# Kernel tuning notes

Hardware: AMD Instinct MI355X
Metric: run time of the kernel (lower is better)

The kernel has to match this reference:

```python
import jax, jax.numpy as jnp
import numpy as np

B, S, DM, DE, H, DH, DC, DCq, DR = 4, 2048, 1024, 1024, 16, 64, 128, 128, 32
SCALE = 1.0 / np.sqrt(DH + DR)


def _rope_tables(seq_len, dim, theta=10000.0):
    inv = 1.0 / (theta ** (jnp.arange(0, dim, 2, dtype=jnp.float32) / dim))  # [dim/2]
    t = jnp.arange(seq_len, dtype=jnp.float32)
    ang = t[:, None] * inv[None, :]  # [S, dim/2]
    return jnp.cos(ang), jnp.sin(ang)


def _apply_rope(xq, xk, cos, sin):
    # xq, xk: [B, S, H, DR]; complex rotary on (even, odd) pairs
    def rot(x):
        s = x.shape
        xr = x.reshape(*s[:-1], s[-1] // 2, 2)
        r, i = xr[..., 0], xr[..., 1]
        c = cos[None, :s[1], None, :]
        sn = sin[None, :s[1], None, :]
        out = jnp.stack([r * c - i * sn, r * sn + i * c], axis=-1)
        return out.reshape(s)
    return rot(xq), rot(xk)


def setup_inputs() -> dict:
    key = jax.random.key(0)
    ks = jax.random.split(key, 10)
    def lin(k, din, dout):
        return 0.02 * jax.random.normal(k, (din, dout), jnp.float32)
    inp = {
        "x": jax.random.normal(ks[0], (B, S, DM), jnp.float32),
        "mask": jnp.tril(jnp.ones((S, S), jnp.float32))[None, None],
        "W_dkv": lin(ks[1], DM, DC),  "b_dkv": jnp.zeros((DC,), jnp.float32),
        "W_dq":  lin(ks[2], DM, DCq), "b_dq":  jnp.zeros((DCq,), jnp.float32),
        "W_uk":  lin(ks[3], DC, DE),  "b_uk":  jnp.zeros((DE,), jnp.float32),
        "W_uv":  lin(ks[4], DC, DE),  "b_uv":  jnp.zeros((DE,), jnp.float32),
        "W_uq":  lin(ks[5], DCq, DE), "b_uq":  jnp.zeros((DE,), jnp.float32),
        "W_qr":  lin(ks[6], DCq, DR * H), "b_qr": jnp.zeros((DR * H,), jnp.float32),
        "W_kr":  lin(ks[7], DM, DR),  "b_kr": jnp.zeros((DR,), jnp.float32),
        "W_o":   lin(ks[8], DE, DM),  "b_o":  jnp.zeros((DM,), jnp.float32),
    }
    return inp


def reference(x, mask, W_dkv, b_dkv, W_dq, b_dq, W_uk, b_uk, W_uv, b_uv,
              W_uq, b_uq, W_qr, b_qr, W_kr, b_kr, W_o, b_o):
    bs, seq_len, _ = x.shape
    cos, sin = _rope_tables(2 * S, DR)

    c_q = x @ W_dq + b_dq            # [B,S,DCq]
    c_kv = x @ W_dkv + b_dkv         # [B,S,DC]
    k_r = x @ W_kr + b_kr            # [B,S,DR]

    q_c = (c_q @ W_uq + b_uq).reshape(bs, seq_len, H, DH)
    k_c = (c_kv @ W_uk + b_uk).reshape(bs, seq_len, H, DH)
    v_c = (c_kv @ W_uv + b_uv).reshape(bs, seq_len, H, DH)

    q_r = (c_q @ W_qr + b_qr).reshape(bs, seq_len, H, DR)
    k_r = jnp.broadcast_to(k_r[:, :, None, :], (bs, seq_len, H, DR))
    q_r, k_r = _apply_rope(q_r, k_r, cos, sin)

    q_t = jnp.concatenate([q_c, q_r], axis=-1)  # [B,S,H,DH+DR]
    k_t = jnp.concatenate([k_c, k_r], axis=-1)

    attn = jnp.einsum('bqhd,bkhd->bhqk', q_t, k_t) * SCALE  # [B,H,S,S]
    m = jnp.where(mask == 0, -jnp.inf, mask)  # faithful masked_fill then add
    attn = attn + m
    p = jax.nn.softmax(attn, axis=-1)
    out = jnp.einsum('bhqk,bkhd->bqhd', p, v_c).reshape(bs, seq_len, H * DH)
    return out @ W_o + b_o
```

## Files before the change

### kernel.cpp

```cpp
#include <hip/hip_runtime.h>
#include <cstdint>
#include <cstddef>

#define S_ 2048
#define B_ 4
#define H_ 16
#define ALPHA_Q 0.14724394f

typedef __attribute__((ext_vector_type(8))) __bf16 bf16x8;
typedef __attribute__((ext_vector_type(4))) __bf16 bf16x4;
typedef __attribute__((ext_vector_type(4))) float f32x4;
typedef __attribute__((ext_vector_type(16))) float f32x16;

__device__ __forceinline__ f32x16 mfma32(bf16x8 a, bf16x8 b, f32x16 c) {
  return __builtin_amdgcn_mfma_f32_32x32x16_bf16(a, b, c, 0, 0, 0);
}

__device__ __forceinline__ void gll16(const void* g, void* l) {
  __builtin_amdgcn_global_load_lds(
      (__attribute__((address_space(1))) void*)(uintptr_t)g,
      (__attribute__((address_space(3))) void*)(uint32_t)(uintptr_t)l,
      16, 0, 0);
}

__device__ __forceinline__ int cvtpk(float lo, float hi) {
  int r;
  asm("v_cvt_pk_bf16_f32 %0, %1, %2" : "=v"(r) : "v"(lo), "v"(hi));
  return r;
}

union PAU { int w[4]; bf16x8 v; };

__device__ __forceinline__ bf16x8 packPA(int hi, float a0, float a1, float a2,
                                         float a3, float b0, float b1, float b2,
                                         float b3) {
  const int Ylo = cvtpk(a0, a1);
  const int Yhi = cvtpk(a2, a3);
  const int Xlo = cvtpk(b0, b1);
  const int Xhi = cvtpk(b2, b3);
  const int t0 = __shfl_xor(hi ? Ylo : Xlo, 32);
  const int t1 = __shfl_xor(hi ? Yhi : Xhi, 32);
  PAU u;
  u.w[0] = hi ? t0 : Ylo;
  u.w[1] = hi ? t1 : Yhi;
  u.w[2] = hi ? Xlo : t0;
  u.w[3] = hi ? Xhi : t1;
  return u.v;
}

__device__ __forceinline__ float tmax16(const f32x16& v) {
  float a[8];
#pragma unroll
  for (int i = 0; i < 8; ++i) a[i] = fmaxf(v[i], v[i + 8]);
#pragma unroll
  for (int s = 4; s > 0; s >>= 1)
#pragma unroll
    for (int i = 0; i < s; ++i) a[i] = fmaxf(a[i], a[i + s]);
  return a[0];
}

__global__ __launch_bounds__(256) void mla_prep(
    const float* __restrict__ x, __bf16* __restrict__ xb,
    const float* __restrict__ W_dq, const float* __restrict__ W_dkv,
    const float* __restrict__ W_kr, const float* __restrict__ W_uq,
    const float* __restrict__ W_qr, const float* __restrict__ W_uk,
    const float* __restrict__ W_uv, const float* __restrict__ W_o,
    __bf16* __restrict__ WdT, __bf16* __restrict__ WuqT,
    __bf16* __restrict__ WukvT, __bf16* __restrict__ WoT,
    const float* __restrict__ b_dq, const float* __restrict__ b_dkv,
    const float* __restrict__ b_kr, const float* __restrict__ b_uq,
    const float* __restrict__ b_qr, const float* __restrict__ b_uk,
    const float* __restrict__ b_uv, float* __restrict__ bias_d,
    float* __restrict__ bias_uq, float* __restrict__ bias_ukv,
    float* __restrict__ ropec, float* __restrict__ ropes) {
  const int id = blockIdx.x;
  const int t = threadIdx.x;
  __shared__ float tile[32][33];

  if (id < 4096) {
    const size_t i = ((size_t)id * 256 + t) * 8;
    float4 a = *(const float4*)&x[i];
    float4 b = *(const float4*)&x[i + 4];
    bf16x8 v;
    v[0] = (__bf16)a.x; v[1] = (__bf16)a.y; v[2] = (__bf16)a.z; v[3] = (__bf16)a.w;
    v[4] = (__bf16)b.x; v[5] = (__bf16)b.y; v[6] = (__bf16)b.z; v[7] = (__bf16)b.w;
    *(bf16x8*)&xb[i] = v;
    return;
  }
  if (id < 5856) {
    int rel = id - 4096;
    const float* W;
    __bf16* WT;
    int K, N, nt;
    if (rel < 128)      { W = W_dq;  WT = WdT;                      K = 1024; N = 128;  nt = 4; }
    else if (rel < 256) { W = W_dkv; WT = WdT + (size_t)128 * 1024; K = 1024; N = 128;  nt = 4;  rel -= 128; }
    else if (rel < 288) { W = W_kr;  WT = WdT + (size_t)256 * 1024; K = 1024; N = 32;   nt = 1;  rel -= 256; }
    else if (rel < 416) { W = W_uq;  WT = WuqT;                     K = 128;  N = 1024; nt = 32; rel -= 288; }
    else if (rel < 480) { W = W_qr;  WT = WuqT + (size_t)1024 * 128; K = 128; N = 512;  nt = 16; rel -= 416; }
    else if (rel < 608) { W = W_uk;  WT = WukvT;                    K = 128;  N = 1024; nt = 32; rel -= 480; }
    else if (rel < 736) { W = W_uv;  WT = WukvT + (size_t)1024 * 128; K = 128; N = 1024; nt = 32; rel -= 608; }
    else                { W = W_o;   WT = WoT;                      K = 1024; N = 1024; nt = 32; rel -= 736; }
    const int n0 = (rel % nt) * 32, k0 = (rel / nt) * 32;
    const int tx = t & 31, ty = t >> 5;
#pragma unroll
    for (int i = 0; i < 32; i += 8)
      tile[ty + i][tx] = W[(size_t)(k0 + ty + i) * N + n0 + tx];
    __syncthreads();
#pragma unroll
    for (int i = 0; i < 32; i += 8)
      WT[(size_t)(n0 + ty + i) * K + k0 + tx] = (__bf16)tile[tx][ty + i];
    return;
  }
  if (id < 5984) {
    const int g = (id - 5856) * 256 + t;
    const int s = g >> 4, i = g & 15;
    const float inv = exp2f(-(float)i * (13.287712379549449f / 16.0f));
    const float ang = (float)s * inv;
    ropec[g] = cosf(ang);
    ropes[g] = sinf(ang);
    return;
  }
  {
    const int g = (id - 5984) * 256 + t;
    if (g < 384)
      bias_d[g] = (g < 128) ? b_dq[g] : (g < 256) ? b_dkv[g - 128]
                 : (g < 288) ? b_kr[g - 256] : 0.f;
    if (g < 1536) bias_uq[g] = (g < 1024) ? b_uq[g] : b_qr[g - 1024];
    if (g < 2048) bias_ukv[g] = (g < 1024) ? b_uk[g] : b_uv[g - 1024];
  }
}

template <int MODE>
__global__ __launch_bounds__(256) void gemm32(
    const __bf16* __restrict__ A, int lda, const __bf16* __restrict__ BT, int ldbt,
    const float* __restrict__ bias, void* __restrict__ C0, void* __restrict__ C1,
    int ldc, int K) {
  const int n0 = blockIdx.x * 128;
  const int m0 = blockIdx.y * 128;
  const int wave = threadIdx.x >> 6, lane = threadIdx.x & 63;
  const int hi = lane >> 5, lq = lane & 31;
  const int wm = (wave >> 1) * 64, wn = (wave & 1) * 64;
  __shared__ __bf16 __attribute__((aligned(16))) ldsA[8 * 128 * 8];
  __shared__ __bf16 __attribute__((aligned(16))) ldsB[8 * 128 * 8];

  const f32x16 fz16 = {0.f, 0.f, 0.f, 0.f, 0.f, 0.f, 0.f, 0.f,
                       0.f, 0.f, 0.f, 0.f, 0.f, 0.f, 0.f, 0.f};
  f32x16 acc00 = fz16, acc01 = fz16, acc10 = fz16, acc11 = fz16;

  for (int k0 = 0; k0 < K; k0 += 64) {
    __syncthreads();
#pragma unroll
    for (int i = 0; i < 8; ++i) {
      const int c = wave * 8 + i;
      if (c < 16) {
        const int sl = c >> 1, half = c & 1;
        gll16(&A[(size_t)(m0 + half * 64 + lane) * lda + k0 + sl * 8],
              &ldsA[(sl * 128 + half * 64) * 8]);
      } else {
        const int cc = c - 16;
        const int sl = cc >> 1, half = cc & 1;
        gll16(&BT[(size_t)(n0 + half * 64 + lane) * ldbt + k0 + sl * 8],
              &ldsB[(sl * 128 + half * 64) * 8]);
      }
    }
    __syncthreads();

#pragma unroll
    for (int ks = 0; ks < 4; ++ks) {
      const int sl = ks * 2 + hi;
      bf16x8 a0 = *(const bf16x8*)&ldsA[(sl * 128 + wm + lq) * 8];
      bf16x8 a1 = *(const bf16x8*)&ldsA[(sl * 128 + wm + 32 + lq) * 8];
      bf16x8 b0 = *(const bf16x8*)&ldsB[(sl * 128 + wn + lq) * 8];
      bf16x8 b1 = *(const bf16x8*)&ldsB[(sl * 128 + wn + 32 + lq) * 8];
      acc00 = mfma32(a0, b0, acc00);
      acc01 = mfma32(a0, b1, acc01);
      acc10 = mfma32(a1, b0, acc10);
      acc11 = mfma32(a1, b1, acc11);
    }
  }

  const f32x16* accs[2][2] = {{&acc00, &acc01}, {&acc10, &acc11}};
#pragma unroll
  for (int ni = 0; ni < 2; ++ni) {
    const int col = n0 + wn + ni * 32 + lq;
    const float bv = bias[col];
#pragma unroll
    for (int mi = 0; mi < 2; ++mi) {
      const f32x16& ac = *accs[mi][ni];
#pragma unroll
      for (int r = 0; r < 16; ++r) {
        const int row = m0 + wm + mi * 32 + (r & 3) + 8 * (r >> 2) + 4 * hi;
        const float v = ac[r] + bv;
        if (MODE == 0) {
          ((__bf16*)C0)[(size_t)row * ldc + col] = (__bf16)v;
        } else if (MODE == 1) {
          ((float*)C0)[(size_t)row * ldc + col] = v;
        } else {
          const int b = row >> 11, s = row & 2047;
          if (col < 1024) {
            const int h = col >> 6, d = col & 63;
            const size_t o = ((size_t)(b * H_ + h) * S_ + s) * 96 + d;
            if (MODE == 2)
              ((__bf16*)C0)[o] = (__bf16)(v * ALPHA_Q);
            else
              ((__bf16*)C0)[o] = (__bf16)v;
          } else {
            if (MODE == 2)
              ((__bf16*)C1)[(size_t)row * 512 + col - 1024] = (__bf16)v;
            else
              ((__bf16*)C1)[(size_t)row * 1024 + col - 1024] = (__bf16)v;
          }
        }
      }
    }
  }
}

__global__ __launch_bounds__(256) void mla_glue(
    const __bf16* __restrict__ qr, const __bf16* __restrict__ cqkvr,
    const float* __restrict__ ropec, const float* __restrict__ ropes,
    __bf16* __restrict__ qt, __bf16* __restrict__ ktb,
    const __bf16* __restrict__ vv, __bf16* __restrict__ vt) {
  __shared__ __bf16 __attribute__((aligned(16))) tile[64][72];
  const int t = threadIdx.x;
  if (blockIdx.x < 8192) {
    const int gid = blockIdx.x * 256 + t;
    const int bs = gid >> 8;
    const int h = (gid >> 4) & 15;
    const int i = gid & 15;
    const int b = bs >> 11, s = bs & 2047;
    const float c = ropec[s * 16 + i], sn = ropes[s * 16 + i];
    const size_t o = ((size_t)(b * H_ + h) * S_ + s) * 96 + 64 + 2 * i;
    {
      const float r = (float)qr[(size_t)bs * 512 + h * 32 + 2 * i];
      const float im = (float)qr[(size_t)bs * 512 + h * 32 + 2 * i + 1];
      qt[o] = (__bf16)((r * c - im * sn) * ALPHA_Q);
      qt[o + 1] = (__bf16)((r * sn + im * c) * ALPHA_Q);
    }
    {
      const float r = (float)cqkvr[(size_t)bs * 384 + 256 + 2 * i];
      const float im = (float)cqkvr[(size_t)bs * 384 + 256 + 2 * i + 1];
      ktb[o] = (__bf16)(r * c - im * sn);
      ktb[o + 1] = (__bf16)(r * sn + im * c);
    }
    return;
  }
  const int bid = blockIdx.x - 8192;
  const int s0 = (bid & 31) * 64;
  const int bh = bid >> 5;
  const int b = bh >> 4, h = bh & 15;
  {
    const int r = t >> 2, c0 = (t & 3) * 16;
    const size_t src = (size_t)(b * S_ + s0 + r) * 1024 + h * 64 + c0;
    bf16x8 u0 = *(const bf16x8*)&vv[src];
    bf16x8 u1 = *(const bf16x8*)&vv[src + 8];
    *(bf16x8*)&tile[r][c0] = u0;
    *(bf16x8*)&tile[r][c0 + 8] = u1;
  }
  __syncthreads();
  {
    const int d = t >> 2, sc0 = (t & 3) * 16;
    bf16x8 w0, w1;
#pragma unroll
    for (int e = 0; e < 8; ++e) {
      w0[e] = tile[sc0 + e][d];
      w1[e] = tile[sc0 + 8 + e][d];
    }
    const size_t dst = ((size_t)bh * 64 + d) * S_ + s0 + sc0;
    *(bf16x8*)&vt[dst] = w0;
    *(bf16x8*)&vt[dst + 8] = w1;
  }
}

__global__ __launch_bounds__(256, 3) void mla_attn(const __bf16* __restrict__ qt,
                                                   const __bf16* __restrict__ kt,
                                                   const __bf16* __restrict__ vt,
                                                   __bf16* __restrict__ ao) {
  const int j = blockIdx.x;
  const int bh = blockIdx.y;
  const int wave = threadIdx.x >> 6, lane = threadIdx.x & 63;
  const int hi = lane >> 5, lq = lane & 31;
  const __bf16* Q = qt + (size_t)bh * S_ * 96;
  const __bf16* Kp = kt + (size_t)bh * S_ * 96;
  const __bf16* Vp = vt + (size_t)bh * 64 * S_;
  const int bb = bh >> 4, h = bh & 15;

  __shared__ __bf16 __attribute__((aligned(16))) kbuf[2][12 * 512];
  __shared__ __bf16 __attribute__((aligned(16))) vbuf[2][8 * 512];

  const f32x16 fz16 = {0.f, 0.f, 0.f, 0.f, 0.f, 0.f, 0.f, 0.f,
                       0.f, 0.f, 0.f, 0.f, 0.f, 0.f, 0.f, 0.f};

  auto stage = [&](int t, int bsel) {
    const int kv0 = t * 64;
#pragma unroll
    for (int i = 0; i < 5; ++i) {
      const int c = wave + 4 * i;
      if (c < 12)
        gll16(&Kp[(size_t)(kv0 + lane) * 96 + c * 8], &kbuf[bsel][c * 512]);
      else
        gll16(&Vp[(size_t)lane * S_ + kv0 + (c - 12) * 8], &vbuf[bsel][(c - 12) * 512]);
    }
  };

  for (int pass = 0; pass < 2; ++pass) {
    const int qblk = pass ? (15 - j) : j;
    const int q0w = qblk * 128 + wave * 32;

    bf16x8 qf[6];
#pragma unroll
    for (int kd = 0; kd < 6; ++kd)
      qf[kd] = *(const bf16x8*)&Q[(size_t)(q0w + lq) * 96 + kd * 16 + hi * 8];

    f32x16 o0 = fz16, o1 = fz16;
    float m = -3.0e38f, L = 0.f;

    const int tEnd = (q0w + 31) >> 6;
    const int tMax = qblk * 2 + 1;

    stage(0, 0);
    __syncthreads();

    int bsel = 0;
    for (int t = 0; t <= tMax; ++t) {
      if (t < tMax) stage(t + 1, bsel ^ 1);
      if (t <= tEnd) {
        f32x16 s0 = fz16, s1 = fz16;
#pragma unroll
        for (int kd = 0; kd < 6; ++kd) {
          const int sl = kd * 2 + hi;
          bf16x8 a0 = *(const bf16x8*)&kbuf[bsel][(sl * 64 + lq) * 8];
          bf16x8 a1 = *(const bf16x8*)&kbuf[bsel][(sl * 64 + 32 + lq) * 8];
          s0 = mfma32(a0, qf[kd], s0);
          s1 = mfma32(a1, qf[kd], s1);
        }
        if (t == tEnd) {
          const int qg = q0w + lq;
          const int kvb = t * 64 + 4 * hi;
#pragma unroll
          for (int r = 0; r < 16; ++r) {
            const int crow = (r & 3) + 8 * (r >> 2);
            if (kvb + crow > qg) s0[r] = -3.0e38f;
            if (kvb + 32 + crow > qg) s1[r] = -3.0e38f;
          }
        }
        float tm = fmaxf(tmax16(s0), tmax16(s1));
        tm = fmaxf(tm, __shfl_xor(tm, 32));
        if (!__all(tm <= m + 8.0f)) {
          const float mnew = fmaxf(m, tm);
          const float sc = exp2f(m - mnew);
          m = mnew;
          L *= sc;
          o0 *= sc;
          o1 *= sc;
        }
        float p0[16], p1[16];
#pragma unroll
        for (int r = 0; r < 16; ++r) {
          p0[r] = exp2f(s0[r] - m);
          p1[r] = exp2f(s1[r] - m);
        }
        float a[16];
#pragma unroll
        for (int r = 0; r < 16; ++r) a[r] = p0[r] + p1[r];
#pragma unroll
        for (int s = 8; s > 0; s >>= 1)
#pragma unroll
          for (int i = 0; i < s; ++i) a[i] += a[i + s];
        float ps = a[0];
        ps += __shfl_xor(ps, 32);
        L += ps;
        bf16x8 pa[4];
        pa[0] = packPA(hi, p0[0], p0[1], p0[2], p0[3], p0[4], p0[5], p0[6], p0[7]);
        pa[1] = packPA(hi, p0[8], p0[9], p0[10], p0[11], p0[12], p0[13], p0[14], p0[15]);
        pa[2] = packPA(hi, p1[0], p1[1], p1[2], p1[3], p1[4], p1[5], p1[6], p1[7]);
        pa[3] = packPA(hi, p1[8], p1[9], p1[10], p1[11], p1[12], p1[13], p1[14], p1[15]);
#pragma unroll
        for (int ks = 0; ks < 4; ++ks) {
          const int sl = ks * 2 + hi;
          bf16x8 v0 = *(const bf16x8*)&vbuf[bsel][(sl * 64 + lq) * 8];
          bf16x8 v1 = *(const bf16x8*)&vbuf[bsel][(sl * 64 + 32 + lq) * 8];
          o0 = mfma32(v0, pa[ks], o0);
          o1 = mfma32(v1, pa[ks], o1);
        }
      }
      __syncthreads();
      bsel ^= 1;
    }

    const float invL = 1.0f / L;
    __bf16* aorow = ao + (size_t)(bb * S_ + q0w + lq) * 1024 + h * 64;
#pragma unroll
    for (int rr = 0; rr < 4; ++rr) {
      bf16x4 w0, w1;
#pragma unroll
      for (int jj = 0; jj < 4; ++jj) {
        w0[jj] = (__bf16)(o0[4 * rr + jj] * invL);
        w1[jj] = (__bf16)(o1[4 * rr + jj] * invL);
      }
      *(bf16x4*)&aorow[rr * 8 + 4 * hi] = w0;
      *(bf16x4*)&aorow[32 + rr * 8 + 4 * hi] = w1;
    }
  }
}

extern "C" void kernel_launch(void* const* d_in, const int* in_sizes, int n_in,
                              void* d_out, int out_size, void* d_ws, size_t ws_size,
                              hipStream_t stream) {
  (void)in_sizes; (void)n_in; (void)out_size; (void)ws_size;
  const float* x = (const float*)d_in[0];
  const float* W_dkv = (const float*)d_in[2];
  const float* b_dkv = (const float*)d_in[3];
  const float* W_dq = (const float*)d_in[4];
  const float* b_dq = (const float*)d_in[5];
  const float* W_uk = (const float*)d_in[6];
  const float* b_uk = (const float*)d_in[7];
  const float* W_uv = (const float*)d_in[8];
  const float* b_uv = (const float*)d_in[9];
  const float* W_uq = (const float*)d_in[10];
  const float* b_uq = (const float*)d_in[11];
  const float* W_qr = (const float*)d_in[12];
  const float* b_qr = (const float*)d_in[13];
  const float* W_kr = (const float*)d_in[14];
  const float* b_kr = (const float*)d_in[15];
  const float* W_o = (const float*)d_in[16];
  const float* b_o = (const float*)d_in[17];
  float* out = (float*)d_out;

  char* ws = (char*)d_ws;
  size_t off = 0;
  auto take = [&](size_t nbytes) -> char* {
    char* p = ws + off;
    off += (nbytes + 255) & ~(size_t)255;
    return p;
  };
  __bf16* xb = (__bf16*)take((size_t)8192 * 1024 * 2);
  __bf16* WdT = (__bf16*)take((size_t)384 * 1024 * 2);
  __bf16* WuqT = (__bf16*)take((size_t)1536 * 128 * 2);
  __bf16* WukvT = (__bf16*)take((size_t)2048 * 128 * 2);
  __bf16* WoT = (__bf16*)take((size_t)1024 * 1024 * 2);
  float* bias_d = (float*)take(384 * 4);
  float* bias_uq = (float*)take(1536 * 4);
  float* bias_ukv = (float*)take(2048 * 4);
  float* ropec = (float*)take((size_t)S_ * 16 * 4);
  float* ropes = (float*)take((size_t)S_ * 16 * 4);
  __bf16* cqkvr = (__bf16*)take((size_t)8192 * 384 * 2);
  __bf16* qr = (__bf16*)take((size_t)8192 * 512 * 2);
  __bf16* vv = (__bf16*)take((size_t)8192 * 1024 * 2);
  __bf16* qt = (__bf16*)take((size_t)B_ * H_ * S_ * 96 * 2);
  __bf16* ktb = (__bf16*)take((size_t)B_ * H_ * S_ * 96 * 2);
  __bf16* vt = (__bf16*)take((size_t)B_ * H_ * 64 * S_ * 2);
  __bf16* aout = (__bf16*)take((size_t)8192 * 1024 * 2);

  hipMemsetAsync(WdT + (size_t)288 * 1024, 0, (size_t)96 * 1024 * 2, stream);

  mla_prep<<<6000, 256, 0, stream>>>(x, xb, W_dq, W_dkv, W_kr, W_uq, W_qr, W_uk,
                                     W_uv, W_o, WdT, WuqT, WukvT, WoT, b_dq,
                                     b_dkv, b_kr, b_uq, b_qr, b_uk, b_uv, bias_d,
                                     bias_uq, bias_ukv, ropec, ropes);

  gemm32<0><<<dim3(3, 64), 256, 0, stream>>>(xb, 1024, WdT, 1024, bias_d,
                                             cqkvr, nullptr, 384, 1024);
  gemm32<2><<<dim3(12, 64), 256, 0, stream>>>(cqkvr, 384, WuqT, 128, bias_uq,
                                              qt, qr, 0, 128);
  gemm32<3><<<dim3(16, 64), 256, 0, stream>>>(cqkvr + 128, 384, WukvT, 128,
                                              bias_ukv, ktb, vv, 0, 128);

  mla_glue<<<8192 + 2048, 256, 0, stream>>>(qr, cqkvr, ropec, ropes, qt, ktb, vv, vt);

  mla_attn<<<dim3(8, 64), 256, 0, stream>>>(qt, ktb, vt, aout);

  gemm32<1><<<dim3(8, 64), 256, 0, stream>>>(aout, 1024, WoT, 1024, b_o, out,
                                             nullptr, 1024, 1024);
}
```

Measured before the change: 341.3 us.

## Merge up-projection GEMMs, reorder attention grid, compute softmax denominators via MFMA

Combines the Q and KV up-projection GEMMs into one launch with block-index dispatch. Swaps the attention grid axes so blocks of the same head/batch are scheduled differently. Staging uses incrementing pointers instead of recomputing addresses. The softmax row-sum is accumulated by an extra MFMA against a ones vector instead of a scalar tree reduction plus shuffle, trading VALU work for extra matrix work.

```diff
diff --git a/kernel.cpp b/kernel.cpp
--- a/kernel.cpp
+++ b/kernel.cpp
@@ -133,8 +133,7 @@
 template <int MODE>
 __global__ __launch_bounds__(256) void gemm32(
     const __bf16* __restrict__ A, int lda, const __bf16* __restrict__ BT, int ldbt,
-    const float* __restrict__ bias, void* __restrict__ C0, void* __restrict__ C1,
-    int ldc, int K) {
+    const float* __restrict__ bias, void* __restrict__ C0, int ldc, int K) {
   const int n0 = blockIdx.x * 128;
   const int m0 = blockIdx.y * 128;
   const int wave = threadIdx.x >> 6, lane = threadIdx.x & 63;
@@ -191,25 +190,93 @@
       for (int r = 0; r < 16; ++r) {
         const int row = m0 + wm + mi * 32 + (r & 3) + 8 * (r >> 2) + 4 * hi;
         const float v = ac[r] + bv;
-        if (MODE == 0) {
+        if (MODE == 0)
           ((__bf16*)C0)[(size_t)row * ldc + col] = (__bf16)v;
-        } else if (MODE == 1) {
+        else
           ((float*)C0)[(size_t)row * ldc + col] = v;
+      }
+    }
+  }
+}
+
+__global__ __launch_bounds__(256) void gemm32up(
+    const __bf16* __restrict__ cqkvr, const __bf16* __restrict__ WuqT,
+    const __bf16* __restrict__ WukvT, const float* __restrict__ bias_uq,
+    const float* __restrict__ bias_ukv, __bf16* __restrict__ qt,
+    __bf16* __restrict__ qr, __bf16* __restrict__ ktb, __bf16* __restrict__ vv) {
+  const bool isQ = blockIdx.x < 12;
+  const int n0 = (isQ ? blockIdx.x : (blockIdx.x - 12)) * 128;
+  const __bf16* A = cqkvr + (isQ ? 0 : 128);
+  const __bf16* BT = isQ ? WuqT : WukvT;
+  const float* bias = isQ ? bias_uq : bias_ukv;
+  const int m0 = blockIdx.y * 128;
+  const int wave = threadIdx.x >> 6, lane = threadIdx.x & 63;
+  const int hi = lane >> 5, lq = lane & 31;
+  const int wm = (wave >> 1) * 64, wn = (wave & 1) * 64;
+  __shared__ __bf16 __attribute__((aligned(16))) ldsA[8 * 128 * 8];
+  __shared__ __bf16 __attribute__((aligned(16))) ldsB[8 * 128 * 8];
+
+  const f32x16 fz16 = {0.f, 0.f, 0.f, 0.f, 0.f, 0.f, 0.f, 0.f,
+                       0.f, 0.f, 0.f, 0.f, 0.f, 0.f, 0.f, 0.f};
+  f32x16 acc00 = fz16, acc01 = fz16, acc10 = fz16, acc11 = fz16;
+
+  for (int k0 = 0; k0 < 128; k0 += 64) {
+    __syncthreads();
+#pragma unroll
+    for (int i = 0; i < 8; ++i) {
+      const int c = wave * 8 + i;
+      if (c < 16) {
+        const int sl = c >> 1, half = c & 1;
+        gll16(&A[(size_t)(m0 + half * 64 + lane) * 384 + k0 + sl * 8],
+              &ldsA[(sl * 128 + half * 64) * 8]);
+      } else {
+        const int cc = c - 16;
+        const int sl = cc >> 1, half = cc & 1;
+        gll16(&BT[(size_t)(n0 + half * 64 + lane) * 128 + k0 + sl * 8],
+              &ldsB[(sl * 128 + half * 64) * 8]);
+      }
+    }
+    __syncthreads();
+
+#pragma unroll
+    for (int ks = 0; ks < 4; ++ks) {
+      const int sl = ks * 2 + hi;
+      bf16x8 a0 = *(const bf16x8*)&ldsA[(sl * 128 + wm + lq) * 8];
+      bf16x8 a1 = *(const bf16x8*)&ldsA[(sl * 128 + wm + 32 + lq) * 8];
+      bf16x8 b0 = *(const bf16x8*)&ldsB[(sl * 128 + wn + lq) * 8];
+      bf16x8 b1 = *(const bf16x8*)&ldsB[(sl * 128 + wn + 32 + lq) * 8];
+      acc00 = mfma32(a0, b0, acc00);
+      acc01 = mfma32(a0, b1, acc01);
+      acc10 = mfma32(a1, b0, acc10);
+      acc11 = mfma32(a1, b1, acc11);
+    }
+  }
+
+  const f32x16* accs[2][2] = {{&acc00, &acc01}, {&acc10, &acc11}};
+#pragma unroll
+  for (int ni = 0; ni < 2; ++ni) {
+    const int col = n0 + wn + ni * 32 + lq;
+    const float bv = bias[col];
+#pragma unroll
+    for (int mi = 0; mi < 2; ++mi) {
+      const f32x16& ac = *accs[mi][ni];
+#pragma unroll
+      for (int r = 0; r < 16; ++r) {
+        const int row = m0 + wm + mi * 32 + (r & 3) + 8 * (r >> 2) + 4 * hi;
+        const float v = ac[r] + bv;
+        const int b = row >> 11, s = row & 2047;
+        if (col < 1024) {
+          const int h = col >> 6, d = col & 63;
+          const size_t o = ((size_t)(b * H_ + h) * S_ + s) * 96 + d;
+          if (isQ)
+            qt[o] = (__bf16)(v * ALPHA_Q);
+          else
+            ktb[o] = (__bf16)v;
         } else {
-          const int b = row >> 11, s = row & 2047;
-          if (col < 1024) {
-            const int h = col >> 6, d = col & 63;
-            const size_t o = ((size_t)(b * H_ + h) * S_ + s) * 96 + d;
-            if (MODE == 2)
-              ((__bf16*)C0)[o] = (__bf16)(v * ALPHA_Q);
-            else
-              ((__bf16*)C0)[o] = (__bf16)v;
-          } else {
-            if (MODE == 2)
-              ((__bf16*)C1)[(size_t)row * 512 + col - 1024] = (__bf16)v;
-            else
-              ((__bf16*)C1)[(size_t)row * 1024 + col - 1024] = (__bf16)v;
-          }
+          if (isQ)
+            qr[(size_t)row * 512 + col - 1024] = (__bf16)v;
+          else
+            vv[(size_t)row * 1024 + col - 1024] = (__bf16)v;
         }
       }
     }
@@ -276,8 +343,8 @@
                                                    const __bf16* __restrict__ kt,
                                                    const __bf16* __restrict__ vt,
                                                    __bf16* __restrict__ ao) {
-  const int j = blockIdx.x;
-  const int bh = blockIdx.y;
+  const int bh = blockIdx.x;
+  const int j = blockIdx.y;
   const int wave = threadIdx.x >> 6, lane = threadIdx.x & 63;
   const int hi = lane >> 5, lq = lane & 31;
   const __bf16* Q = qt + (size_t)bh * S_ * 96;
@@ -290,18 +357,9 @@
 
   const f32x16 fz16 = {0.f, 0.f, 0.f, 0.f, 0.f, 0.f, 0.f, 0.f,
                        0.f, 0.f, 0.f, 0.f, 0.f, 0.f, 0.f, 0.f};
-
-  auto stage = [&](int t, int bsel) {
-    const int kv0 = t * 64;
-#pragma unroll
-    for (int i = 0; i < 5; ++i) {
-      const int c = wave + 4 * i;
-      if (c < 12)
-        gll16(&Kp[(size_t)(kv0 + lane) * 96 + c * 8], &kbuf[bsel][c * 512]);
-      else
-        gll16(&Vp[(size_t)lane * S_ + kv0 + (c - 12) * 8], &vbuf[bsel][(c - 12) * 512]);
-    }
-  };
+  bf16x8 onesA;
+#pragma unroll
+  for (int e = 0; e < 8; ++e) onesA[e] = (__bf16)1.0f;
 
   for (int pass = 0; pass < 2; ++pass) {
     const int qblk = pass ? (15 - j) : j;
@@ -312,18 +370,39 @@
     for (int kd = 0; kd < 6; ++kd)
       qf[kd] = *(const bf16x8*)&Q[(size_t)(q0w + lq) * 96 + kd * 16 + hi * 8];
 
-    f32x16 o0 = fz16, o1 = fz16;
-    float m = -3.0e38f, L = 0.f;
+    f32x16 o0 = fz16, o1 = fz16, Lacc = fz16;
+    float m = -3.0e38f;
 
     const int tEnd = (q0w + 31) >> 6;
     const int tMax = qblk * 2 + 1;
 
-    stage(0, 0);
+    const __bf16* gsrc[5];
+#pragma unroll
+    for (int i = 0; i < 5; ++i) {
+      const int c = wave + 4 * i;
+      gsrc[i] = (c < 12) ? Kp + (size_t)lane * 96 + c * 8
+                         : Vp + (size_t)lane * S_ + (c - 12) * 8;
+    }
+    auto stage = [&](int bsel) {
+#pragma unroll
+      for (int i = 0; i < 5; ++i) {
+        const int c = wave + 4 * i;
+        if (c < 12) {
+          gll16(gsrc[i], &kbuf[bsel][c * 512]);
+          gsrc[i] += 64 * 96;
+        } else {
+          gll16(gsrc[i], &vbuf[bsel][(c - 12) * 512]);
+          gsrc[i] += 64;
+        }
+      }
+    };
+
+    stage(0);
     __syncthreads();
 
     int bsel = 0;
     for (int t = 0; t <= tMax; ++t) {
-      if (t < tMax) stage(t + 1, bsel ^ 1);
+      if (t < tMax) stage(bsel ^ 1);
       if (t <= tEnd) {
         f32x16 s0 = fz16, s1 = fz16;
 #pragma unroll
@@ -350,7 +429,7 @@
           const float mnew = fmaxf(m, tm);
           const float sc = exp2f(m - mnew);
           m = mnew;
-          L *= sc;
+          Lacc[0] *= sc;
           o0 *= sc;
           o1 *= sc;
         }
@@ -360,16 +439,6 @@
           p0[r] = exp2f(s0[r] - m);
           p1[r] = exp2f(s1[r] - m);
         }
-        float a[16];
-#pragma unroll
-        for (int r = 0; r < 16; ++r) a[r] = p0[r] + p1[r];
-#pragma unroll
-        for (int s = 8; s > 0; s >>= 1)
-#pragma unroll
-          for (int i = 0; i < s; ++i) a[i] += a[i + s];
-        float ps = a[0];
-        ps += __shfl_xor(ps, 32);
-        L += ps;
         bf16x8 pa[4];
         pa[0] = packPA(hi, p0[0], p0[1], p0[2], p0[3], p0[4], p0[5], p0[6], p0[7]);
         pa[1] = packPA(hi, p0[8], p0[9], p0[10], p0[11], p0[12], p0[13], p0[14], p0[15]);
@@ -382,13 +451,14 @@
           bf16x8 v1 = *(const bf16x8*)&vbuf[bsel][(sl * 64 + 32 + lq) * 8];
           o0 = mfma32(v0, pa[ks], o0);
           o1 = mfma32(v1, pa[ks], o1);
+          Lacc = mfma32(onesA, pa[ks], Lacc);
         }
       }
       __syncthreads();
       bsel ^= 1;
     }
 
-    const float invL = 1.0f / L;
+    const float invL = 1.0f / Lacc[0];
     __bf16* aorow = ao + (size_t)(bb * S_ + q0w + lq) * 1024 + h * 64;
 #pragma unroll
     for (int rr = 0; rr < 4; ++rr) {
@@ -460,16 +530,14 @@
                                      bias_uq, bias_ukv, ropec, ropes);
 
   gemm32<0><<<dim3(3, 64), 256, 0, stream>>>(xb, 1024, WdT, 1024, bias_d,
-                                             cqkvr, nullptr, 384, 1024);
-  gemm32<2><<<dim3(12, 64), 256, 0, stream>>>(cqkvr, 384, WuqT, 128, bias_uq,
-                                              qt, qr, 0, 128);
-  gemm32<3><<<dim3(16, 64), 256, 0, stream>>>(cqkvr + 128, 384, WukvT, 128,
-                                              bias_ukv, ktb, vv, 0, 128);
+                                             cqkvr, 384, 1024);
+  gemm32up<<<dim3(28, 64), 256, 0, stream>>>(cqkvr, WuqT, WukvT, bias_uq,
+                                             bias_ukv, qt, qr, ktb, vv);
 
   mla_glue<<<8192 + 2048, 256, 0, stream>>>(qr, cqkvr, ropec, ropes, qt, ktb, vv, vt);
 
-  mla_attn<<<dim3(8, 64), 256, 0, stream>>>(qt, ktb, vt, aout);
+  mla_attn<<<dim3(64, 8), 256, 0, stream>>>(qt, ktb, vt, aout);
 
   gemm32<1><<<dim3(8, 64), 256, 0, stream>>>(aout, 1024, WoT, 1024, b_o, out,
-                                             nullptr, 1024, 1024);
-}
+                                             1024, 1024);
+}
```

Result: no change. 339.9 us (-0.4%).
